# Optimization experiments

Measured on AMD Instinct MI355X. Metric: run time of the kernel, lower is better.

## Reference

```python
import jax, jax.numpy as jnp
import numpy as np

B_IMG, T_PER, DIN = 8, 4096, 1176
D, E, BN, L, TOP_K, OUT = 1024, 8, 64, 4, 2, 4096


def setup_inputs() -> dict:
    key = jax.random.key(0)
    ks = jax.random.split(key, 16)
    s = 0.02
    inp = {
        "pixel_values": jax.random.normal(ks[0], (B_IMG * T_PER, DIN), jnp.float32),
        "image_grid_thw": jnp.tile(jnp.array([[1, 64, 64]], dtype=jnp.int64), (B_IMG, 1)),
        # in_proj (no bias)
        "w_in": jax.random.normal(ks[1], (DIN, D), jnp.float32) * s,
        # skin classifier: Linear(D,64) -> ReLU -> Linear(64,3)
        "w_sc1": jax.random.normal(ks[2], (D, 64), jnp.float32) * s,
        "b_sc1": jnp.zeros((64,), jnp.float32),
        "w_sc2": jax.random.normal(ks[3], (64, 3), jnp.float32) * s,
        "b_sc2": jnp.zeros((3,), jnp.float32),
        # per-adapter-layer routers (stacked over L)
        "w_rimg": jax.random.normal(ks[4], (L, D, E), jnp.float32) * s,
        "w_rskin": jax.random.normal(ks[5], (L, 3, E), jnp.float32) * s,
        # per-layer, per-expert MLP: Linear(D,BN) -> ReLU -> Linear(BN,D)
        "ew1": jax.random.normal(ks[6], (L, E, D, BN), jnp.float32) * s,
        "eb1": jnp.zeros((L, E, BN), jnp.float32),
        "ew2": jax.random.normal(ks[7], (L, E, BN, D), jnp.float32) * s,
        "eb2": jnp.zeros((L, E, D), jnp.float32),
        # out_proj
        "w_out": jax.random.normal(ks[8], (D, OUT), jnp.float32) * s,
        "b_out": jnp.zeros((OUT,), jnp.float32),
    }
    return inp


def _forward(pixel_values, image_grid_thw, w_in, w_sc1, b_sc1, w_sc2, b_sc2,
             w_rimg, w_rskin, ew1, eb1, ew2, eb2, w_out, b_out):
    B = image_grid_thw.shape[0]
    T = pixel_values.shape[0] // B  # equal chunk sizes (t*h*w identical per image)
    x = pixel_values.reshape(B, T, -1)

    def per_image(xc):  # xc: [T, din]
        h = xc @ w_in  # [T, D]
        g = h.mean(0)
        skin_logits = jax.nn.relu(g @ w_sc1 + b_sc1) @ w_sc2 + b_sc2  # [3]
        skin_probs = jax.nn.softmax(skin_logits)

        def layer(carry, params):
            h, aux = carry
            wri, wrs, W1, B1, W2, B2 = params
            logits = h @ wri + skin_probs @ wrs  # [T, E]
            probs = jax.nn.softmax(logits, axis=-1)
            tp, ti = jax.lax.top_k(probs, TOP_K)
            tp = tp / (tp.sum(-1, keepdims=True) + 1e-6)
            rows = jnp.arange(h.shape[0])[:, None]
            # dense per-token expert weights (0 for non-selected experts)
            wfull = jnp.zeros_like(probs).at[rows, ti].add(tp)
            mask = jnp.zeros_like(probs).at[rows, ti].add(1.0)
            h1 = jax.nn.relu(jnp.einsum('td,edb->teb', h, W1) + B1)  # [T,E,BN]
            h2 = jnp.einsum('teb,ebd->ted', h1, W2) + B2             # [T,E,D]
            moe_out = jnp.einsum('ted,te->td', h2, wfull)
            aux = aux + (probs.mean(0) * mask.mean(0)).sum() * probs.shape[-1]
            return (h + moe_out, aux), None

        (h, aux), _ = jax.lax.scan(layer, (h, jnp.zeros((), h.dtype)),
                                   (w_rimg, w_rskin, ew1, eb1, ew2, eb2))
        return h.mean(0), skin_logits, aux

    pooled, skin_logits, aux = jax.vmap(per_image)(x)
    vision_proj = pooled @ w_out + b_out
    return pooled, vision_proj, aux.sum(), skin_logits


def reference(pixel_values, image_grid_thw, w_in, w_sc1, b_sc1, w_sc2, b_sc2,
              w_rimg, w_rskin, ew1, eb1, ew2, eb2, w_out, b_out):
    return _forward(pixel_values, image_grid_thw, w_in, w_sc1, b_sc1, w_sc2, b_sc2,
                    w_rimg, w_rskin, ew1, eb1, ew2, eb2, w_out, b_out)
```

## Files before the change

### kernel.cpp

```cpp
#include <hip/hip_runtime.h>
#include <math.h>

#define TPI  4096
#define TT   32768
#define DIN  1176
#define KP   1184
#define DM   1024
#define NE   8
#define BN   64
#define NL   4
#define DOUT 4096

typedef __attribute__((ext_vector_type(4))) float floatx4;
typedef __attribute__((ext_vector_type(8))) short bf16x8;
typedef unsigned int uint;

__device__ inline short f2bf(float x) {
    unsigned u = __float_as_uint(x);
    u += 0x7fffu + ((u >> 16) & 1u);
    return (short)(u >> 16);
}
__device__ inline float bf2f(short h) {
    return __uint_as_float(((unsigned)(unsigned short)h) << 16);
}

#define GLP(p) ((const __attribute__((address_space(1))) void*)(p))
#define LDSP(p) ((__attribute__((address_space(3))) void*)(p))
#define ASYNC16(g, s) __builtin_amdgcn_global_load_lds(GLP(g), LDSP(s), 16, 0, 0)

#define OFF_H0    0ul
#define OFF_H1    67108864ul
#define OFF_XB    134217728ul
#define OFF_WBT   211812352ul
#define OFF_E1T   214237184ul
#define OFF_E2T   218431488ul
#define OFF_BTOK  222625792ul
#define OFF_BW1   222756864ul
#define OFF_BW2   222887936ul
#define OFF_T2E   223019008ul
#define OFF_T2W   223150080ul
#define OFF_WQ    223412224ul
#define OFF_Z     223416320ul
#define Z_BYTES   39232ul
#define OFF_RB    223455552ul
#define OFF_WRT   223456576ul

__global__ __launch_bounds__(256) void convx_kernel(
    const float* __restrict__ X, short* __restrict__ Xb)
{
    const long row = blockIdx.x;
    const float* src = X + row * (long)DIN;
    short* dst = Xb + row * (long)KP;
    for (int i = threadIdx.x; i < 296; i += 256) {
        short4 s;
        if (i < 294) {
            float4 v = *(const float4*)(src + i * 4);
            s.x = f2bf(v.x); s.y = f2bf(v.y); s.z = f2bf(v.z); s.w = f2bf(v.w);
        } else {
            s.x = 0; s.y = 0; s.z = 0; s.w = 0;
        }
        *(short4*)(dst + i * 4) = s;
    }
}

__global__ __launch_bounds__(256) void transp_kernel(
    const float* __restrict__ src, short* __restrict__ dst, int RS, int CS, int DK)
{
    __shared__ float tb[64][65];
    const int kt = blockIdx.x * 64, nt = blockIdx.y * 64;
    const long sb = (long)blockIdx.z * RS * CS;
    const long db = (long)blockIdx.z * CS * DK;
    const int rr = threadIdx.x >> 6, cc = threadIdx.x & 63;
#pragma unroll
    for (int i = 0; i < 16; ++i) {
        int r = i * 4 + rr;
        int k = kt + r, n = nt + cc;
        tb[r][cc] = (k < RS && n < CS) ? src[sb + (long)k * CS + n] : 0.0f;
    }
    __syncthreads();
#pragma unroll
    for (int i = 0; i < 16; ++i) {
        int r = i * 4 + rr;
        int n = nt + r, k = kt + cc;
        if (n < CS && k < DK) dst[db + (long)n * DK + k] = f2bf(tb[cc][r]);
    }
}

__global__ __launch_bounds__(256) void wrt_kernel(
    const float* __restrict__ w_rimg, short* __restrict__ wrT)
{
    const int l = blockIdx.x >> 4, e = blockIdx.x & 15;
    short* dst = wrT + ((long)l * 16 + e) * 1024;
    if (e < 8) {
        const float* src = w_rimg + (long)l * 8192 + e;
        for (int k = threadIdx.x; k < 1024; k += 256) dst[k] = f2bf(src[k * 8]);
    } else {
        for (int k = threadIdx.x; k < 1024; k += 256) dst[k] = 0;
    }
}

__global__ __launch_bounds__(256) void gemm_in_mfma(
    const short* __restrict__ Xb, const short* __restrict__ Wbt, short* __restrict__ Hb)
{
    __shared__ __align__(16) short As[128 * 32];
    __shared__ __align__(16) short Bs[128 * 32];
    const int tid = threadIdx.x;
    const int m0 = blockIdx.x * 128, n0 = blockIdx.y * 128;
    const int w = tid >> 6, lane = tid & 63;
    const int quad = lane >> 4, l15 = lane & 15;
    const int wm = (w >> 1) * 64, wn = (w & 1) * 64;

    floatx4 acc[4][4];
#pragma unroll
    for (int i = 0; i < 4; ++i)
#pragma unroll
        for (int j = 0; j < 4; ++j) acc[i][j] = 0.0f;

    const int r0 = tid >> 2, kof = (tid & 3) * 8;
    const int r1 = (tid + 256) >> 2;
    const short* a0p = Xb + (long)(m0 + r0) * KP + kof;
    const short* a1p = Xb + (long)(m0 + r1) * KP + kof;
    const short* b0p = Wbt + (long)(n0 + r0) * KP + kof;
    const short* b1p = Wbt + (long)(n0 + r1) * KP + kof;
    short* as0 = As + tid * 8;
    short* as1 = As + (tid + 256) * 8;
    short* bs0 = Bs + tid * 8;
    short* bs1 = Bs + (tid + 256) * 8;

    for (int k0 = 0; k0 < KP; k0 += 32) {
        __syncthreads();
        ASYNC16(a0p + k0, as0);
        ASYNC16(a1p + k0, as1);
        ASYNC16(b0p + k0, bs0);
        ASYNC16(b1p + k0, bs1);
        __syncthreads();
        bf16x8 af[4], bfr[4];
#pragma unroll
        for (int i = 0; i < 4; ++i)
            af[i] = *(const bf16x8*)&As[(wm + i * 16 + l15) * 32 + quad * 8];
#pragma unroll
        for (int j = 0; j < 4; ++j)
            bfr[j] = *(const bf16x8*)&Bs[(wn + j * 16 + l15) * 32 + quad * 8];
#pragma unroll
        for (int i = 0; i < 4; ++i)
#pragma unroll
            for (int j = 0; j < 4; ++j)
                acc[i][j] = __builtin_amdgcn_mfma_f32_16x16x32_bf16(af[i], bfr[j], acc[i][j], 0, 0, 0);
    }
#pragma unroll
    for (int i = 0; i < 4; ++i)
#pragma unroll
        for (int j = 0; j < 4; ++j)
#pragma unroll
            for (int r = 0; r < 4; ++r)
                Hb[(long)(m0 + wm + i * 16 + quad * 4 + r) * DM + n0 + wn + j * 16 + l15] =
                    f2bf(acc[i][j][r]);
}

__global__ __launch_bounds__(256) void colmean_kernel(
    const short* __restrict__ Hb, float* __restrict__ outp)
{
    const int col = blockIdx.x * 256 + threadIdx.x;
    const int img = blockIdx.y;
    const int t0 = blockIdx.z * 256;
    const short* p = Hb + ((long)img * TPI + t0) * DM + col;
    float s = 0.0f;
#pragma unroll 8
    for (int t = 0; t < 256; ++t) s += bf2f(p[(long)t * DM]);
    atomicAdd(&outp[img * DM + col], s * (1.0f / 4096.0f));
}

__global__ __launch_bounds__(256) void skin1_kernel(
    const float* __restrict__ g, const float* __restrict__ w_sc1,
    const float* __restrict__ b_sc1, float* __restrict__ hsg)
{
    __shared__ float red[4][64];
    const int img = blockIdx.x;
    const int part = threadIdx.x >> 6, c = threadIdx.x & 63;
    float s = 0.0f;
    for (int i = 0; i < 256; ++i) {
        int d = part * 256 + i;
        s += g[img * DM + d] * w_sc1[d * 64 + c];
    }
    red[part][c] = s;
    __syncthreads();
    if (part == 0) {
        float v = red[0][c] + red[1][c] + red[2][c] + red[3][c] + b_sc1[c];
        hsg[img * 64 + c] = fmaxf(v, 0.0f);
    }
}

__global__ __launch_bounds__(256) void skin2_kernel(
    const float* __restrict__ hsg, const float* __restrict__ w_sc2, const float* __restrict__ b_sc2,
    const float* __restrict__ w_rskin, float* __restrict__ skin_logits_out, float* __restrict__ rb)
{
    __shared__ float l3[24];
    __shared__ float sp[24];
    const int tid = threadIdx.x;
    if (tid < 24) {
        int img = tid / 3, j = tid % 3;
        float s = b_sc2[j];
        for (int c = 0; c < 64; ++c) s += hsg[img * 64 + c] * w_sc2[c * 3 + j];
        l3[tid] = s;
        skin_logits_out[tid] = s;
    }
    __syncthreads();
    if (tid < 8) {
        float v0 = l3[tid * 3], v1 = l3[tid * 3 + 1], v2 = l3[tid * 3 + 2];
        float m = fmaxf(v0, fmaxf(v1, v2));
        float e0 = expf(v0 - m), e1 = expf(v1 - m), e2 = expf(v2 - m);
        float inv = 1.0f / (e0 + e1 + e2);
        sp[tid * 3] = e0 * inv; sp[tid * 3 + 1] = e1 * inv; sp[tid * 3 + 2] = e2 * inv;
    }
    __syncthreads();
    {
        int l = tid >> 6, img = (tid >> 3) & 7, e = tid & 7;
        float s = 0.0f;
#pragma unroll
        for (int c = 0; c < 3; ++c) s += sp[img * 3 + c] * w_rskin[(l * 3 + c) * 8 + e];
        rb[tid] = s;
    }
}

__global__ __launch_bounds__(256) void router_kernel(
    const short* __restrict__ Hb, const short* __restrict__ wrT, const float* __restrict__ rb,
    uint* __restrict__ top2e, float* __restrict__ top2w, int* __restrict__ counts_pair,
    float* __restrict__ sum_probs, float* __restrict__ mask_cnt, int l)
{
    __shared__ __align__(16) short As[8 * 64 * 32];
    __shared__ float lgS[64 * 9];
    const int tid = threadIdx.x;
    const int tok0 = blockIdx.x * 64;
    const int img = tok0 >> 12;
    const int w = tid >> 6, lane = tid & 63;
    const int quad = lane >> 4, l15 = lane & 15;

    const short* rowptr = Hb + (long)(tok0 + w * 16 + (lane >> 2)) * DM + (lane & 3) * 8;
    short* sdst = As + tid * 8;
    const short* wrl = wrT + (long)l * 16 * 1024 + l15 * 1024 + quad * 8;

    floatx4 acc = 0.0f;
    for (int k0 = 0; k0 < DM; k0 += 256) {
        __syncthreads();
#pragma unroll
        for (int c = 0; c < 8; ++c) ASYNC16(rowptr + k0 + c * 32, sdst + c * 2048);
        __syncthreads();
#pragma unroll
        for (int c = 0; c < 8; ++c) {
            bf16x8 af = *(const bf16x8*)&As[c * 2048 + (w * 16 + l15) * 32 + quad * 8];
            bf16x8 bf = *(const bf16x8*)(wrl + k0 + c * 32);
            acc = __builtin_amdgcn_mfma_f32_16x16x32_bf16(af, bf, acc, 0, 0, 0);
        }
    }
    if (l15 < 8) {
#pragma unroll
        for (int r = 0; r < 4; ++r) lgS[(w * 16 + quad * 4 + r) * 9 + l15] = acc[r];
    }
    __syncthreads();

    if (tid < 64) {
        const int token = tok0 + tid;
        float p[8];
        float mx = -1e30f;
#pragma unroll
        for (int e = 0; e < 8; ++e) {
            float v = lgS[tid * 9 + e] + rb[l * 64 + img * 8 + e];
            p[e] = v; mx = fmaxf(mx, v);
        }
        float s = 0.0f;
#pragma unroll
        for (int e = 0; e < 8; ++e) { p[e] = expf(p[e] - mx); s += p[e]; }
        float inv = 1.0f / s;
#pragma unroll
        for (int e = 0; e < 8; ++e) p[e] *= inv;

        int i1 = 0; float b1v = p[0];
#pragma unroll
        for (int e = 1; e < 8; ++e) if (p[e] > b1v) { b1v = p[e]; i1 = e; }
        int i2 = -1; float b2v = -1.0f;
#pragma unroll
        for (int e = 0; e < 8; ++e) if (e != i1 && p[e] > b2v) { b2v = p[e]; i2 = e; }
        float den = b1v + b2v + 1e-6f;
        top2e[token] = (uint)i1 | ((uint)i2 << 8);
        top2w[2 * token] = b1v / den;
        top2w[2 * token + 1] = b2v / den;

        atomicAdd(&counts_pair[l * 64 + i1 * 8 + i2], 1);

        for (int slot = 0; slot < 2; ++slot) {
            int esel = slot ? i2 : i1;
#pragma unroll
            for (int e = 0; e < 8; ++e) {
                unsigned long long m = __ballot(esel == e);
                int pc = __popcll(m);
                if (pc && tid == (__ffsll(m) - 1))
                    atomicAdd(&mask_cnt[l * 64 + img * 8 + e], (float)pc);
            }
        }
#pragma unroll
        for (int e = 0; e < 8; ++e) {
            float r = p[e];
            for (int off = 32; off > 0; off >>= 1) r += __shfl_down(r, off);
            if (tid == 0) atomicAdd(&sum_probs[l * 64 + img * 8 + e], r);
        }
    }
}

__global__ __launch_bounds__(64) void wq_kernel(
    const int* __restrict__ counts_pair, int* __restrict__ wq, int* __restrict__ nworkp,
    int* __restrict__ pair_off, int l)
{
    const int p = threadIdx.x;
    int cnt = counts_pair[l * 64 + p];
    int x = cnt;
    for (int off = 1; off < 64; off <<= 1) {
        int y = __shfl_up(x, off);
        if (p >= off) x += y;
    }
    pair_off[p] = x - cnt;
    int nb = (cnt + 63) >> 6;
    int t = nb;
    for (int off = 1; off < 64; off <<= 1) {
        int y = __shfl_up(t, off);
        if (p >= off) t += y;
    }
    int start = t - nb;
    for (int i = 0; i < nb; ++i) wq[start + i] = p | ((i * 64) << 6);
    if (p == 63) nworkp[0] = t;
}

__global__ __launch_bounds__(256) void scatter_kernel(
    const uint* __restrict__ top2e, const float* __restrict__ top2w,
    const int* __restrict__ pair_off, int* __restrict__ cursors,
    int* __restrict__ btok, float* __restrict__ bw1, float* __restrict__ bw2, int l)
{
    const int t = blockIdx.x * 256 + threadIdx.x;
    const int lane = threadIdx.x & 63;
    uint pe = top2e[t];
    int p = (int)(pe & 255u) * 8 + (int)((pe >> 8) & 255u);
    float w1 = top2w[2 * t], w2 = top2w[2 * t + 1];
    int myoff = pair_off[p];
    unsigned long long rem = __ballot(true);
    while (rem) {
        int leader = __ffsll(rem) - 1;
        int pv = __shfl(p, leader);
        unsigned long long m = __ballot(p == pv);
        int basep = 0;
        if (lane == leader) basep = atomicAdd(&cursors[l * 64 + pv], __popcll(m));
        basep = __shfl(basep, leader);
        if (p == pv) {
            int pos = basep + __popcll(m & ((1ull << lane) - 1ull));
            int s = myoff + pos;
            btok[s] = t;
            bw1[s] = w1;
            bw2[s] = w2;
        }
        rem &= ~m;
    }
}

__global__ __launch_bounds__(256) void expert_pair(
    const short* __restrict__ Hin, short* __restrict__ Hout,
    const int* __restrict__ counts_pair, const int* __restrict__ pair_off,
    const int* __restrict__ btok, const float* __restrict__ bw1, const float* __restrict__ bw2,
    const short* __restrict__ ew1t, const float* __restrict__ eb1,
    const short* __restrict__ ew2t, const float* __restrict__ eb2,
    const int* __restrict__ wq, const int* __restrict__ nworkp, int l)
{
    __shared__ __align__(16) short As[8 * 64 * 32];
    __shared__ __align__(16) short h1a[64 * 72];
    __shared__ __align__(16) short h1b[64 * 72];
    __shared__ int tkS[64];
    __shared__ float w1S[64], w2S[64];

    const int tid = threadIdx.x;
    const int w = tid >> 6, lane = tid & 63;
    const int quad = lane >> 4, l15 = lane & 15;
    const int nwork = nworkp[0];
    short* sdst = As + tid * 8;

    for (int wi = blockIdx.x; wi < nwork; wi += gridDim.x) {
        const int item = wq[wi];
        const int p = item & 63, base = item >> 6;
        const int ea = p >> 3, eb = p & 7;
        const int off = pair_off[p];
        const int cnt = counts_pair[l * 64 + p];

        __syncthreads();
        if (tid < 64) {
            bool valid = (base + tid) < cnt;
            int s = off + base + tid;
            tkS[tid] = valid ? btok[s] : 0;
            w1S[tid] = valid ? bw1[s] : 0.0f;
            w2S[tid] = valid ? bw2[s] : 0.0f;
        }
        __syncthreads();
        const int lea = l * 8 + ea, leb = l * 8 + eb;
        const short* rowptr = Hin + (long)tkS[w * 16 + (lane >> 2)] * DM + (lane & 3) * 8;

        floatx4 acc1a[4], acc1b[4];
#pragma unroll
        for (int i = 0; i < 4; ++i) { acc1a[i] = 0.0f; acc1b[i] = 0.0f; }
        const short* w1ap = ew1t + ((long)lea * 64 + w * 16 + l15) * DM + quad * 8;
        const short* w1bp = ew1t + ((long)leb * 64 + w * 16 + l15) * DM + quad * 8;

        for (int k0 = 0; k0 < DM; k0 += 256) {
            __syncthreads();
#pragma unroll
            for (int c = 0; c < 8; ++c) ASYNC16(rowptr + k0 + c * 32, sdst + c * 2048);
            __syncthreads();
#pragma unroll
            for (int c = 0; c < 8; ++c) {
                bf16x8 ba = *(const bf16x8*)(w1ap + k0 + c * 32);
                bf16x8 bb = *(const bf16x8*)(w1bp + k0 + c * 32);
#pragma unroll
                for (int i = 0; i < 4; ++i) {
                    bf16x8 af = *(const bf16x8*)&As[c * 2048 + (i * 16 + l15) * 32 + quad * 8];
                    acc1a[i] = __builtin_amdgcn_mfma_f32_16x16x32_bf16(af, ba, acc1a[i], 0, 0, 0);
                    acc1b[i] = __builtin_amdgcn_mfma_f32_16x16x32_bf16(af, bb, acc1b[i], 0, 0, 0);
                }
            }
        }
        {
            float b1av = eb1[lea * BN + w * 16 + l15];
            float b1bv = eb1[leb * BN + w * 16 + l15];
#pragma unroll
            for (int i = 0; i < 4; ++i)
#pragma unroll
                for (int r = 0; r < 4; ++r) {
                    h1a[(i * 16 + quad * 4 + r) * 72 + w * 16 + l15] =
                        f2bf(fmaxf(acc1a[i][r] + b1av, 0.0f));
                    h1b[(i * 16 + quad * 4 + r) * 72 + w * 16 + l15] =
                        f2bf(fmaxf(acc1b[i][r] + b1bv, 0.0f));
                }
        }
        __syncthreads();

        const short* w2ap = ew2t + ((long)lea * DM + w * 16 + l15) * 64 + quad * 8;
        const short* w2bp = ew2t + ((long)leb * DM + w * 16 + l15) * 64 + quad * 8;
        const bool rowvalid = (base + (tid >> 2)) < cnt;
        const long orow = (long)tkS[tid >> 2] * DM;

        for (int gidx = 0; gidx < 4; ++gidx) {
            const int g0 = gidx * 256;
#pragma unroll
            for (int c = 0; c < 8; ++c) ASYNC16(rowptr + g0 + c * 32, sdst + c * 2048);
            __syncthreads();
#pragma unroll
            for (int ns = 0; ns < 4; ++ns) {
                const int n0 = g0 + ns * 64;
                floatx4 a2a[4], a2b[4];
#pragma unroll
                for (int tj = 0; tj < 4; ++tj) { a2a[tj] = 0.0f; a2b[tj] = 0.0f; }
#pragma unroll
                for (int kk = 0; kk < 2; ++kk) {
                    bf16x8 wa = *(const bf16x8*)(w2ap + (long)n0 * 64 + kk * 32);
                    bf16x8 wb = *(const bf16x8*)(w2bp + (long)n0 * 64 + kk * 32);
#pragma unroll
                    for (int tj = 0; tj < 4; ++tj) {
                        bf16x8 ha = *(const bf16x8*)&h1a[(tj * 16 + l15) * 72 + kk * 32 + quad * 8];
                        bf16x8 hb = *(const bf16x8*)&h1b[(tj * 16 + l15) * 72 + kk * 32 + quad * 8];
                        a2a[tj] = __builtin_amdgcn_mfma_f32_16x16x32_bf16(wa, ha, a2a[tj], 0, 0, 0);
                        a2b[tj] = __builtin_amdgcn_mfma_f32_16x16x32_bf16(wb, hb, a2b[tj], 0, 0, 0);
                    }
                }
                const int nloc = ns * 64 + w * 16 + quad * 4;
                const int csub = nloc >> 5, cidx = nloc & 31;
                float4 b2av = *(const float4*)&eb2[lea * DM + g0 + nloc];
                float4 b2bv = *(const float4*)&eb2[leb * DM + g0 + nloc];
#pragma unroll
                for (int tj = 0; tj < 4; ++tj) {
                    int tk = tj * 16 + l15;
                    float w1 = w1S[tk], w2 = w2S[tk];
                    short* slot = &As[csub * 2048 + tk * 32 + cidx];
                    short4 res = *(short4*)slot;
                    short4 o;
                    o.x = f2bf(bf2f(res.x) + w1 * (a2a[tj][0] + b2av.x) + w2 * (a2b[tj][0] + b2bv.x));
                    o.y = f2bf(bf2f(res.y) + w1 * (a2a[tj][1] + b2av.y) + w2 * (a2b[tj][1] + b2bv.y));
                    o.z = f2bf(bf2f(res.z) + w1 * (a2a[tj][2] + b2av.z) + w2 * (a2b[tj][2] + b2bv.z));
                    o.w = f2bf(bf2f(res.w) + w1 * (a2a[tj][3] + b2av.w) + w2 * (a2b[tj][3] + b2bv.w));
                    *(short4*)slot = o;
                }
            }
            __syncthreads();
            if (rowvalid) {
                const int tok = tid >> 2;
#pragma unroll
                for (int c2 = 0; c2 < 2; ++c2) {
                    const int csub = (tid & 3) * 2 + c2;
#pragma unroll
                    for (int j = 0; j < 4; ++j) {
                        int4 v = *(const int4*)&As[csub * 2048 + tok * 32 + j * 8];
                        *(int4*)(Hout + orow + g0 + csub * 32 + j * 8) = v;
                    }
                }
            }
            __syncthreads();
        }
    }
}

__global__ __launch_bounds__(256) void vproj_kernel(
    const float* __restrict__ pooled, const float* __restrict__ w_out,
    const float* __restrict__ b_out, float* __restrict__ outp)
{
    __shared__ float ps[8 * 128];
    const int tid = threadIdx.x;
    const int n = blockIdx.x * 256 + tid;
    const int d0 = blockIdx.y * 128;
#pragma unroll
    for (int i = 0; i < 4; ++i) {
        int idx = tid + i * 256;
        ps[idx] = pooled[(idx >> 7) * DM + d0 + (idx & 127)];
    }
    __syncthreads();
    float acc[8];
    float binit = (blockIdx.y == 0) ? b_out[n] : 0.0f;
#pragma unroll
    for (int img = 0; img < 8; ++img) acc[img] = binit;
    for (int d = 0; d < 128; ++d) {
        float wv = w_out[(long)(d0 + d) * DOUT + n];
#pragma unroll
        for (int img = 0; img < 8; ++img) acc[img] += ps[img * 128 + d] * wv;
    }
#pragma unroll
    for (int img = 0; img < 8; ++img) atomicAdd(&outp[img * DOUT + n], acc[img]);
}

__global__ __launch_bounds__(64) void aux_kernel(
    const float* __restrict__ sum_probs, const float* __restrict__ mask_cnt,
    float* __restrict__ outp)
{
    const int tid = threadIdx.x;
    float v = 0.0f;
    if (tid < 32) {
        float s = 0.0f;
#pragma unroll
        for (int e = 0; e < 8; ++e) s += sum_probs[tid * 8 + e] * mask_cnt[tid * 8 + e];
        v = s * (8.0f / (4096.0f * 4096.0f));
    }
    for (int off = 32; off > 0; off >>= 1) v += __shfl_down(v, off);
    if (tid == 0) outp[0] = v;
}

extern "C" void kernel_launch(void* const* d_in, const int* in_sizes, int n_in,
                              void* d_out, int out_size, void* d_ws, size_t ws_size,
                              hipStream_t stream) {
    const float* X       = (const float*)d_in[0];
    const float* w_in    = (const float*)d_in[2];
    const float* w_sc1   = (const float*)d_in[3];
    const float* b_sc1   = (const float*)d_in[4];
    const float* w_sc2   = (const float*)d_in[5];
    const float* b_sc2   = (const float*)d_in[6];
    const float* w_rimg  = (const float*)d_in[7];
    const float* w_rskin = (const float*)d_in[8];
    const float* ew1     = (const float*)d_in[9];
    const float* eb1     = (const float*)d_in[10];
    const float* ew2     = (const float*)d_in[11];
    const float* eb2     = (const float*)d_in[12];
    const float* w_out   = (const float*)d_in[13];
    const float* b_out   = (const float*)d_in[14];

    float* out = (float*)d_out;
    char* ws = (char*)d_ws;

    short* H0   = (short*)(ws + OFF_H0);
    short* H1   = (short*)(ws + OFF_H1);
    short* Xb   = (short*)(ws + OFF_XB);
    short* Wbt  = (short*)(ws + OFF_WBT);
    short* ew1t = (short*)(ws + OFF_E1T);
    short* ew2t = (short*)(ws + OFF_E2T);
    int*   btok = (int*)(ws + OFF_BTOK);
    float* bw1  = (float*)(ws + OFF_BW1);
    float* bw2  = (float*)(ws + OFF_BW2);
    uint*  top2e = (uint*)(ws + OFF_T2E);
    float* top2w = (float*)(ws + OFF_T2W);
    int*   wq    = (int*)(ws + OFF_WQ);
    int*   counts_pair = (int*)(ws + OFF_Z);
    int*   cursors     = (int*)(ws + OFF_Z + 1024);
    int*   nworkp      = (int*)(ws + OFF_Z + 2048);
    int*   pair_off    = (int*)(ws + OFF_Z + 2112);
    float* sum_probs   = (float*)(ws + OFF_Z + 2368);
    float* mask_cnt    = (float*)(ws + OFF_Z + 3392);
    float* g           = (float*)(ws + OFF_Z + 4416);
    float* hsg         = (float*)(ws + OFF_Z + 37184);
    float* rb          = (float*)(ws + OFF_RB);
    short* wrT         = (short*)(ws + OFF_WRT);

    hipMemsetAsync(d_out, 0, (size_t)out_size * sizeof(float), stream);
    hipMemsetAsync(ws + OFF_Z, 0, Z_BYTES, stream);

    dim3 b256(256);
    convx_kernel<<<TT, b256, 0, stream>>>(X, Xb);
    transp_kernel<<<dim3(19, 16, 1), b256, 0, stream>>>(w_in, Wbt, DIN, DM, KP);
    transp_kernel<<<dim3(16, 1, 32), b256, 0, stream>>>(ew1, ew1t, DM, BN, DM);
    transp_kernel<<<dim3(1, 16, 32), b256, 0, stream>>>(ew2, ew2t, BN, DM, BN);
    wrt_kernel<<<64, b256, 0, stream>>>(w_rimg, wrT);
    gemm_in_mfma<<<dim3(256, 8), b256, 0, stream>>>(Xb, Wbt, H0);
    colmean_kernel<<<dim3(4, 8, 16), b256, 0, stream>>>(H0, g);
    skin1_kernel<<<8, b256, 0, stream>>>(g, w_sc1, b_sc1, hsg);
    skin2_kernel<<<1, b256, 0, stream>>>(hsg, w_sc2, b_sc2, w_rskin, out + 40961, rb);

    short* Hc = H0;
    short* Hn = H1;
    for (int l = 0; l < NL; ++l) {
        router_kernel<<<512, b256, 0, stream>>>(Hc, wrT, rb, top2e, top2w,
                                                counts_pair, sum_probs, mask_cnt, l);
        wq_kernel<<<1, 64, 0, stream>>>(counts_pair, wq, nworkp, pair_off, l);
        scatter_kernel<<<128, b256, 0, stream>>>(top2e, top2w, pair_off, cursors,
                                                 btok, bw1, bw2, l);
        expert_pair<<<576, b256, 0, stream>>>(Hc, Hn, counts_pair, pair_off, btok, bw1, bw2,
                                              ew1t, eb1, ew2t, eb2, wq, nworkp, l);
        short* tmp = Hc; Hc = Hn; Hn = tmp;
    }
    colmean_kernel<<<dim3(4, 8, 16), b256, 0, stream>>>(Hc, out);
    vproj_kernel<<<dim3(16, 8), b256, 0, stream>>>(out, w_out, b_out, out + 8192);
    aux_kernel<<<1, 64, 0, stream>>>(sum_probs, mask_cnt, out + 40960);
}
```

Baseline: 1.494 ms.

## Fuse next-layer routing into expert kernel, colmean into input GEMM, drop wq kernel

The input GEMM now uses a 64-wide K tile with XOR-swizzled LDS and computes the per-image column mean in its epilogue via atomics, which removes the separate colmean pass. The per-layer work-queue kernel is removed: the scatter and expert kernels each recompute the prefix sums from counts in shared memory. The router for layers 1-3 is fused into the expert kernel, which runs MFMA on the freshly written output tile to produce the next layer's top-2 selections and aux statistics, so a full re-read of H per layer is avoided. KP padding grows to 1216 and the workspace layout is compacted. Costs include a linear pair search per work item, extra LDS and register pressure, and more atomics.

```diff
diff --git a/kernel.cpp b/kernel.cpp
--- a/kernel.cpp
+++ b/kernel.cpp
@@ -4,7 +4,7 @@
 #define TPI  4096
 #define TT   32768
 #define DIN  1176
-#define KP   1184
+#define KP   1216
 #define DM   1024
 #define NE   8
 #define BN   64
@@ -30,20 +30,19 @@
 
 #define OFF_H0    0ul
 #define OFF_H1    67108864ul
-#define OFF_XB    134217728ul
-#define OFF_WBT   211812352ul
-#define OFF_E1T   214237184ul
-#define OFF_E2T   218431488ul
-#define OFF_BTOK  222625792ul
-#define OFF_BW1   222756864ul
-#define OFF_BW2   222887936ul
-#define OFF_T2E   223019008ul
-#define OFF_T2W   223150080ul
-#define OFF_WQ    223412224ul
-#define OFF_Z     223416320ul
+#define OFF_XB    67108864ul
+#define OFF_WBT   146800640ul
+#define OFF_E1T   149291008ul
+#define OFF_E2T   153485312ul
+#define OFF_BTOK  157679616ul
+#define OFF_BW1   157810688ul
+#define OFF_BW2   157941760ul
+#define OFF_T2E   158072832ul
+#define OFF_T2W   158203904ul
+#define OFF_Z     158466048ul
 #define Z_BYTES   39232ul
-#define OFF_RB    223455552ul
-#define OFF_WRT   223456576ul
+#define OFF_RB    158505280ul
+#define OFF_WRT   158506304ul
 
 __global__ __launch_bounds__(256) void convx_kernel(
     const float* __restrict__ X, short* __restrict__ Xb)
@@ -51,7 +50,7 @@
     const long row = blockIdx.x;
     const float* src = X + row * (long)DIN;
     short* dst = Xb + row * (long)KP;
-    for (int i = threadIdx.x; i < 296; i += 256) {
+    for (int i = threadIdx.x; i < 304; i += 256) {
         short4 s;
         if (i < 294) {
             float4 v = *(const float4*)(src + i * 4);
@@ -100,10 +99,11 @@
 }
 
 __global__ __launch_bounds__(256) void gemm_in_mfma(
-    const short* __restrict__ Xb, const short* __restrict__ Wbt, short* __restrict__ Hb)
-{
-    __shared__ __align__(16) short As[128 * 32];
-    __shared__ __align__(16) short Bs[128 * 32];
+    const short* __restrict__ Xb, const short* __restrict__ Wbt,
+    short* __restrict__ Hb, float* __restrict__ g)
+{
+    __shared__ __align__(16) short As[128 * 64];
+    __shared__ __align__(16) short Bs[128 * 64];
     const int tid = threadIdx.x;
     const int m0 = blockIdx.x * 128, n0 = blockIdx.y * 128;
     const int w = tid >> 6, lane = tid & 63;
@@ -116,45 +116,55 @@
 #pragma unroll
         for (int j = 0; j < 4; ++j) acc[i][j] = 0.0f;
 
-    const int r0 = tid >> 2, kof = (tid & 3) * 8;
-    const int r1 = (tid + 256) >> 2;
-    const short* a0p = Xb + (long)(m0 + r0) * KP + kof;
-    const short* a1p = Xb + (long)(m0 + r1) * KP + kof;
-    const short* b0p = Wbt + (long)(n0 + r0) * KP + kof;
-    const short* b1p = Wbt + (long)(n0 + r1) * KP + kof;
-    short* as0 = As + tid * 8;
-    short* as1 = As + (tid + 256) * 8;
-    short* bs0 = Bs + tid * 8;
-    short* bs1 = Bs + (tid + 256) * 8;
-
-    for (int k0 = 0; k0 < KP; k0 += 32) {
+    const int r = tid >> 3;
+    const int gofs = ((tid & 7) ^ (r & 7)) * 8;
+    const short* ap = Xb + (long)(m0 + r) * KP + gofs;
+    const short* bp = Wbt + (long)(n0 + r) * KP + gofs;
+    short* asd = As + tid * 8;
+    short* bsd = Bs + tid * 8;
+    const int rx = l15 & 7;
+
+    for (int k0 = 0; k0 < KP; k0 += 64) {
         __syncthreads();
-        ASYNC16(a0p + k0, as0);
-        ASYNC16(a1p + k0, as1);
-        ASYNC16(b0p + k0, bs0);
-        ASYNC16(b1p + k0, bs1);
+#pragma unroll
+        for (int i = 0; i < 4; ++i) {
+            ASYNC16(ap + (long)i * 32 * KP + k0, asd + i * 2048);
+            ASYNC16(bp + (long)i * 32 * KP + k0, bsd + i * 2048);
+        }
         __syncthreads();
-        bf16x8 af[4], bfr[4];
+#pragma unroll
+        for (int kk = 0; kk < 2; ++kk) {
+            bf16x8 af[4], bfr[4];
+#pragma unroll
+            for (int i = 0; i < 4; ++i)
+                af[i] = *(const bf16x8*)&As[(wm + i * 16 + l15) * 64 + (((kk * 4 + quad)) ^ rx) * 8];
+#pragma unroll
+            for (int j = 0; j < 4; ++j)
+                bfr[j] = *(const bf16x8*)&Bs[(wn + j * 16 + l15) * 64 + (((kk * 4 + quad)) ^ rx) * 8];
+#pragma unroll
+            for (int i = 0; i < 4; ++i)
+#pragma unroll
+                for (int j = 0; j < 4; ++j)
+                    acc[i][j] = __builtin_amdgcn_mfma_f32_16x16x32_bf16(af[i], bfr[j], acc[i][j], 0, 0, 0);
+        }
+    }
+    const int img = m0 >> 12;
+#pragma unroll
+    for (int j = 0; j < 4; ++j) {
+        float cs = 0.0f;
 #pragma unroll
         for (int i = 0; i < 4; ++i)
-            af[i] = *(const bf16x8*)&As[(wm + i * 16 + l15) * 32 + quad * 8];
-#pragma unroll
-        for (int j = 0; j < 4; ++j)
-            bfr[j] = *(const bf16x8*)&Bs[(wn + j * 16 + l15) * 32 + quad * 8];
-#pragma unroll
-        for (int i = 0; i < 4; ++i)
-#pragma unroll
-            for (int j = 0; j < 4; ++j)
-                acc[i][j] = __builtin_amdgcn_mfma_f32_16x16x32_bf16(af[i], bfr[j], acc[i][j], 0, 0, 0);
-    }
-#pragma unroll
-    for (int i = 0; i < 4; ++i)
-#pragma unroll
-        for (int j = 0; j < 4; ++j)
-#pragma unroll
-            for (int r = 0; r < 4; ++r)
-                Hb[(long)(m0 + wm + i * 16 + quad * 4 + r) * DM + n0 + wn + j * 16 + l15] =
-                    f2bf(acc[i][j][r]);
+#pragma unroll
+            for (int r2 = 0; r2 < 4; ++r2) {
+                short hv = f2bf(acc[i][j][r2]);
+                Hb[(long)(m0 + wm + i * 16 + quad * 4 + r2) * DM + n0 + wn + j * 16 + l15] = hv;
+                cs += bf2f(hv);
+            }
+        cs += __shfl_xor(cs, 16);
+        cs += __shfl_xor(cs, 32);
+        if (quad == 0)
+            atomicAdd(&g[img * DM + n0 + wn + j * 16 + l15], cs * (1.0f / 4096.0f));
+    }
 }
 
 __global__ __launch_bounds__(256) void colmean_kernel(
@@ -299,47 +309,37 @@
         }
 #pragma unroll
         for (int e = 0; e < 8; ++e) {
-            float r = p[e];
-            for (int off = 32; off > 0; off >>= 1) r += __shfl_down(r, off);
-            if (tid == 0) atomicAdd(&sum_probs[l * 64 + img * 8 + e], r);
-        }
-    }
-}
-
-__global__ __launch_bounds__(64) void wq_kernel(
-    const int* __restrict__ counts_pair, int* __restrict__ wq, int* __restrict__ nworkp,
-    int* __restrict__ pair_off, int l)
-{
-    const int p = threadIdx.x;
-    int cnt = counts_pair[l * 64 + p];
-    int x = cnt;
-    for (int off = 1; off < 64; off <<= 1) {
-        int y = __shfl_up(x, off);
-        if (p >= off) x += y;
-    }
-    pair_off[p] = x - cnt;
-    int nb = (cnt + 63) >> 6;
-    int t = nb;
-    for (int off = 1; off < 64; off <<= 1) {
-        int y = __shfl_up(t, off);
-        if (p >= off) t += y;
-    }
-    int start = t - nb;
-    for (int i = 0; i < nb; ++i) wq[start + i] = p | ((i * 64) << 6);
-    if (p == 63) nworkp[0] = t;
+            float rsum = p[e];
+            for (int off = 32; off > 0; off >>= 1) rsum += __shfl_down(rsum, off);
+            if (tid == 0) atomicAdd(&sum_probs[l * 64 + img * 8 + e], rsum);
+        }
+    }
 }
 
 __global__ __launch_bounds__(256) void scatter_kernel(
     const uint* __restrict__ top2e, const float* __restrict__ top2w,
-    const int* __restrict__ pair_off, int* __restrict__ cursors,
+    const int* __restrict__ counts_pair, int* __restrict__ cursors,
     int* __restrict__ btok, float* __restrict__ bw1, float* __restrict__ bw2, int l)
 {
-    const int t = blockIdx.x * 256 + threadIdx.x;
-    const int lane = threadIdx.x & 63;
+    __shared__ int pofS[64];
+    const int tid = threadIdx.x;
+    if (tid < 64) {
+        int c = counts_pair[l * 64 + tid];
+        int x = c;
+#pragma unroll
+        for (int off = 1; off < 64; off <<= 1) {
+            int y = __shfl_up(x, off);
+            if (tid >= off) x += y;
+        }
+        pofS[tid] = x - c;
+    }
+    __syncthreads();
+    const int t = blockIdx.x * 256 + tid;
+    const int lane = tid & 63;
     uint pe = top2e[t];
     int p = (int)(pe & 255u) * 8 + (int)((pe >> 8) & 255u);
     float w1 = top2w[2 * t], w2 = top2w[2 * t + 1];
-    int myoff = pair_off[p];
+    int myoff = pofS[p];
     unsigned long long rem = __ballot(true);
     while (rem) {
         int leader = __ffsll(rem) - 1;
@@ -361,30 +361,59 @@
 
 __global__ __launch_bounds__(256) void expert_pair(
     const short* __restrict__ Hin, short* __restrict__ Hout,
-    const int* __restrict__ counts_pair, const int* __restrict__ pair_off,
+    int* __restrict__ counts_pair,
     const int* __restrict__ btok, const float* __restrict__ bw1, const float* __restrict__ bw2,
     const short* __restrict__ ew1t, const float* __restrict__ eb1,
     const short* __restrict__ ew2t, const float* __restrict__ eb2,
-    const int* __restrict__ wq, const int* __restrict__ nworkp, int l)
+    const short* __restrict__ wrT, const float* __restrict__ rb,
+    uint* __restrict__ top2e, float* __restrict__ top2w,
+    float* __restrict__ sum_probs, float* __restrict__ mask_cnt, int l)
 {
     __shared__ __align__(16) short As[8 * 64 * 32];
     __shared__ __align__(16) short h1a[64 * 72];
     __shared__ __align__(16) short h1b[64 * 72];
     __shared__ int tkS[64];
     __shared__ float w1S[64], w2S[64];
+    __shared__ int pofS[64], cntS[64], tpS[64];
+    __shared__ int nworkS;
+    __shared__ float spLDS[64], mkLDS[64];
 
     const int tid = threadIdx.x;
     const int w = tid >> 6, lane = tid & 63;
     const int quad = lane >> 4, l15 = lane & 15;
-    const int nwork = nworkp[0];
     short* sdst = As + tid * 8;
 
+    if (tid < 64) {
+        int c = counts_pair[l * 64 + tid];
+        cntS[tid] = c;
+        int x = c;
+#pragma unroll
+        for (int off = 1; off < 64; off <<= 1) {
+            int y = __shfl_up(x, off);
+            if (tid >= off) x += y;
+        }
+        pofS[tid] = x - c;
+        int nb = (c + 63) >> 6;
+        int t = nb;
+#pragma unroll
+        for (int off = 1; off < 64; off <<= 1) {
+            int y = __shfl_up(t, off);
+            if (tid >= off) t += y;
+        }
+        tpS[tid] = t;
+        if (tid == 63) nworkS = t;
+    }
+    __syncthreads();
+    const int nwork = nworkS;
+
     for (int wi = blockIdx.x; wi < nwork; wi += gridDim.x) {
-        const int item = wq[wi];
-        const int p = item & 63, base = item >> 6;
+        int p = 0;
+        while (p < 63 && tpS[p] <= wi) ++p;
+        const int cnt = cntS[p];
+        const int nbp = (cnt + 63) >> 6;
+        const int base = (wi - (tpS[p] - nbp)) * 64;
         const int ea = p >> 3, eb = p & 7;
-        const int off = pair_off[p];
-        const int cnt = counts_pair[l * 64 + p];
+        const int off = pofS[p];
 
         __syncthreads();
         if (tid < 64) {
@@ -393,6 +422,8 @@
             tkS[tid] = valid ? btok[s] : 0;
             w1S[tid] = valid ? bw1[s] : 0.0f;
             w2S[tid] = valid ? bw2[s] : 0.0f;
+            spLDS[tid] = 0.0f;
+            mkLDS[tid] = 0.0f;
         }
         __syncthreads();
         const int lea = l * 8 + ea, leb = l * 8 + eb;
@@ -440,6 +471,10 @@
         const short* w2bp = ew2t + ((long)leb * DM + w * 16 + l15) * 64 + quad * 8;
         const bool rowvalid = (base + (tid >> 2)) < cnt;
         const long orow = (long)tkS[tid >> 2] * DM;
+
+        floatx4 acc_lg[4];
+#pragma unroll
+        for (int tf = 0; tf < 4; ++tf) acc_lg[tf] = 0.0f;
 
         for (int gidx = 0; gidx < 4; ++gidx) {
             const int g0 = gidx * 256;
@@ -483,6 +518,19 @@
                 }
             }
             __syncthreads();
+
+            if (l < 3) {
+                const short* wrp = wrT + ((long)(l + 1) * 16 + l15) * 1024 + g0 + w * 64 + quad * 8;
+#pragma unroll
+                for (int kk = 0; kk < 2; ++kk) {
+                    bf16x8 wf = *(const bf16x8*)(wrp + kk * 32);
+#pragma unroll
+                    for (int tf = 0; tf < 4; ++tf) {
+                        bf16x8 of = *(const bf16x8*)&As[(w * 2 + kk) * 2048 + (tf * 16 + l15) * 32 + quad * 8];
+                        acc_lg[tf] = __builtin_amdgcn_mfma_f32_16x16x32_bf16(wf, of, acc_lg[tf], 0, 0, 0);
+                    }
+                }
+            }
             if (rowvalid) {
                 const int tok = tid >> 2;
 #pragma unroll
@@ -496,6 +544,57 @@
                 }
             }
             __syncthreads();
+        }
+
+        if (l < 3) {
+            float* lgF = (float*)As;
+#pragma unroll
+            for (int tf = 0; tf < 4; ++tf)
+                *(floatx4*)&lgF[(w * 64 + tf * 16 + l15) * 16 + quad * 4] = acc_lg[tf];
+            __syncthreads();
+            if (tid < 64) {
+                const bool valid = (base + tid) < cnt;
+                const int token = tkS[tid];
+                const int img = token >> 12;
+                float pb[8]; float mx = -1e30f;
+#pragma unroll
+                for (int e = 0; e < 8; ++e) {
+                    float v = lgF[tid * 16 + e] + lgF[(64 + tid) * 16 + e]
+                            + lgF[(128 + tid) * 16 + e] + lgF[(192 + tid) * 16 + e]
+                            + rb[(l + 1) * 64 + img * 8 + e];
+                    pb[e] = v; mx = fmaxf(mx, v);
+                }
+                float s = 0.0f;
+#pragma unroll
+                for (int e = 0; e < 8; ++e) { pb[e] = expf(pb[e] - mx); s += pb[e]; }
+                float inv = 1.0f / s;
+#pragma unroll
+                for (int e = 0; e < 8; ++e) pb[e] *= inv;
+                int i1 = 0; float b1v = pb[0];
+#pragma unroll
+                for (int e = 1; e < 8; ++e) if (pb[e] > b1v) { b1v = pb[e]; i1 = e; }
+                int i2 = -1; float b2v = -1.0f;
+#pragma unroll
+                for (int e = 0; e < 8; ++e) if (e != i1 && pb[e] > b2v) { b2v = pb[e]; i2 = e; }
+                if (valid) {
+                    float den = b1v + b2v + 1e-6f;
+                    top2e[token] = (uint)i1 | ((uint)i2 << 8);
+                    top2w[2 * token] = b1v / den;
+                    top2w[2 * token + 1] = b2v / den;
+                    atomicAdd(&counts_pair[(l + 1) * 64 + i1 * 8 + i2], 1);
+#pragma unroll
+                    for (int e = 0; e < 8; ++e) atomicAdd(&spLDS[img * 8 + e], pb[e]);
+                    atomicAdd(&mkLDS[img * 8 + i1], 1.0f);
+                    atomicAdd(&mkLDS[img * 8 + i2], 1.0f);
+                }
+            }
+            __syncthreads();
+            if (tid < 64) {
+                float v = spLDS[tid];
+                if (v != 0.0f) atomicAdd(&sum_probs[(l + 1) * 64 + tid], v);
+                float mz = mkLDS[tid];
+                if (mz != 0.0f) atomicAdd(&mask_cnt[(l + 1) * 64 + tid], mz);
+            }
         }
     }
 }
@@ -575,11 +674,8 @@
     float* bw2  = (float*)(ws + OFF_BW2);
     uint*  top2e = (uint*)(ws + OFF_T2E);
     float* top2w = (float*)(ws + OFF_T2W);
-    int*   wq    = (int*)(ws + OFF_WQ);
     int*   counts_pair = (int*)(ws + OFF_Z);
     int*   cursors     = (int*)(ws + OFF_Z + 1024);
-    int*   nworkp      = (int*)(ws + OFF_Z + 2048);
-    int*   pair_off    = (int*)(ws + OFF_Z + 2112);
     float* sum_probs   = (float*)(ws + OFF_Z + 2368);
     float* mask_cnt    = (float*)(ws + OFF_Z + 3392);
     float* g           = (float*)(ws + OFF_Z + 4416);
@@ -596,21 +692,20 @@
     transp_kernel<<<dim3(16, 1, 32), b256, 0, stream>>>(ew1, ew1t, DM, BN, DM);
     transp_kernel<<<dim3(1, 16, 32), b256, 0, stream>>>(ew2, ew2t, BN, DM, BN);
     wrt_kernel<<<64, b256, 0, stream>>>(w_rimg, wrT);
-    gemm_in_mfma<<<dim3(256, 8), b256, 0, stream>>>(Xb, Wbt, H0);
-    colmean_kernel<<<dim3(4, 8, 16), b256, 0, stream>>>(H0, g);
+    gemm_in_mfma<<<dim3(256, 8), b256, 0, stream>>>(Xb, Wbt, H0, g);
     skin1_kernel<<<8, b256, 0, stream>>>(g, w_sc1, b_sc1, hsg);
     skin2_kernel<<<1, b256, 0, stream>>>(hsg, w_sc2, b_sc2, w_rskin, out + 40961, rb);
+    router_kernel<<<512, b256, 0, stream>>>(H0, wrT, rb, top2e, top2w,
+                                            counts_pair, sum_probs, mask_cnt, 0);
 
     short* Hc = H0;
     short* Hn = H1;
     for (int l = 0; l < NL; ++l) {
-        router_kernel<<<512, b256, 0, stream>>>(Hc, wrT, rb, top2e, top2w,
-                                                counts_pair, sum_probs, mask_cnt, l);
-        wq_kernel<<<1, 64, 0, stream>>>(counts_pair, wq, nworkp, pair_off, l);
-        scatter_kernel<<<128, b256, 0, stream>>>(top2e, top2w, pair_off, cursors,
+        scatter_kernel<<<128, b256, 0, stream>>>(top2e, top2w, counts_pair, cursors,
                                                  btok, bw1, bw2, l);
-        expert_pair<<<576, b256, 0, stream>>>(Hc, Hn, counts_pair, pair_off, btok, bw1, bw2,
-                                              ew1t, eb1, ew2t, eb2, wq, nworkp, l);
+        expert_pair<<<576, b256, 0, stream>>>(Hc, Hn, counts_pair, btok, bw1, bw2,
+                                              ew1t, eb1, ew2t, eb2, wrT, rb,
+                                              top2e, top2w, sum_probs, mask_cnt, l);
         short* tmp = Hc; Hc = Hn; Hn = tmp;
     }
     colmean_kernel<<<dim3(4, 8, 16), b256, 0, stream>>>(Hc, out);
```

Measured after the change: 1.419 ms. 5.1% less time.
